# Kernel tuning notes

Hardware: AMD Instinct MI355X
Metric: run time of the kernel (lower is better)

Reference implementation:

```python
import jax, jax.numpy as jnp
import numpy as np

HEADS = 4


def setup_inputs() -> dict:
    key = jax.random.key(0)
    ks = jax.random.split(key, 6)
    b, c, d, h, w = 4, 512, 16, 16, 16
    x = jax.random.normal(ks[0], (b, c, d, h, w), dtype=jnp.float32)
    s = 0.02  # param init scale
    Wq = jax.random.normal(ks[1], (c, c), dtype=jnp.float32) * s
    Wk = jax.random.normal(ks[2], (c, c), dtype=jnp.float32) * s
    Wv = jax.random.normal(ks[3], (c, c), dtype=jnp.float32) * s
    Wproj = jax.random.normal(ks[4], (c, c), dtype=jnp.float32) * s
    bproj = jnp.zeros((c,), dtype=jnp.float32)
    return {"x": x, "Wq": Wq, "Wk": Wk, "Wv": Wv, "Wproj": Wproj, "bproj": bproj}


def reference(x, Wq, Wk, Wv, Wproj, bproj):
    b, c, d, h, w = x.shape
    N = d * h * w
    scale = (c // HEADS) ** -0.5  # module uses ch//heads for scale
    xf = x.reshape(b, c, N)  # (b, c, N)
    # 1x1 Conv1d == channel matmul
    q = jnp.einsum('oc,bcn->bon', Wq, xf)
    k = jnp.einsum('oc,bcn->bon', Wk, xf)
    v = jnp.einsum('oc,bcn->bon', Wv, xf)
    # Faithful to original (buggy) view: split SEQUENCE dim by heads -> (b, H, c, N//H)
    q = q.reshape(b, HEADS, c, N // HEADS)
    k = k.reshape(b, HEADS, c, N // HEADS)
    v = v.reshape(b, HEADS, c, N // HEADS)
    attn = jax.nn.softmax(jnp.einsum('bhqe,bhke->bhqk', q, k) * scale, axis=-1)
    out = jnp.einsum('bhqk,bhke->bhqe', attn, v)  # (b, H, c, N//H)
    out = jnp.swapaxes(out, 2, 3).reshape(b, c, N)  # matches transpose(2,3).view
    out = jnp.einsum('oc,bcn->bon', Wproj, out) + bproj[None, :, None]
    return out.reshape(b, c, d, h, w) + x
```

## Files before the change

kernel.cpp:

```cpp
#include <hip/hip_runtime.h>
#include <stdint.h>


typedef __attribute__((ext_vector_type(8))) short short8;
typedef __attribute__((ext_vector_type(4))) float f32x4;

typedef const __attribute__((address_space(1))) unsigned int* gas_ptr;
typedef __attribute__((address_space(3))) unsigned int* las_ptr;

#define ATTN_SCALE 0.08838834764831845f

__device__ __forceinline__ unsigned short f2bf(float f) {
    union { float f; unsigned int u; } c; c.f = f;
    unsigned int u = c.u;
    u += 0x7fffu + ((u >> 16) & 1u);
    return (unsigned short)(u >> 16);
}

__device__ __forceinline__ void gl_lds16(const void* g, void* l) {
    __builtin_amdgcn_global_load_lds((gas_ptr)(uintptr_t)g, (las_ptr)(uintptr_t)l,
                                     16, 0, 0);
}

template<int LDA, int LDB, int KDIM, bool PERMB = false>
__device__ __forceinline__ void mfma_core(
    const unsigned short* __restrict__ A,
    const unsigned short* __restrict__ B,
    int m0, int n0,
    unsigned short* __restrict__ sA, unsigned short* __restrict__ sB,
    f32x4 acc[4][4])
{
    const int tid  = threadIdx.x;
    const int lane = tid & 63, wave = tid >> 6;
    const int lr = lane >> 2, lc = lane & 3;
    const int lcs = lc ^ ((lr >> 1) & 3);
    const int wm = (wave & 1) * 64, wn = (wave >> 1) * 64;
    const int col = lane & 15, quad = lane >> 4;
    const int swz = (quad ^ ((col >> 1) & 3)) * 8;

    const unsigned short* ga = A + (size_t)(m0 + 32 * wave + lr) * LDA + lcs * 8;
    int rb0 = n0 + 32 * wave + lr;
    int rb1 = rb0 + 16;
    if (PERMB) {
        rb0 = 4 * (rb0 & 127) + (rb0 >> 7);
        rb1 = 4 * (rb1 & 127) + (rb1 >> 7);
    }
    const unsigned short* gb0 = B + (size_t)rb0 * LDB + lcs * 8;
    const unsigned short* gb1 = B + (size_t)rb1 * LDB + lcs * 8;

    const int wr0 = (32 * wave) * 32;
    const int wr1 = (32 * wave + 16) * 32;

    gl_lds16(ga,            sA + wr0);
    gl_lds16(ga + 16 * LDA, sA + wr1);
    gl_lds16(gb0,           sB + wr0);
    gl_lds16(gb1,           sB + wr1);

    constexpr int NK = KDIM / 32;
    for (int kk = 0; kk < NK; ++kk) {
        const int bo = (kk & 1) * 4096;
        if (kk + 1 < NK) {
            const int nb = ((kk + 1) & 1) * 4096;
            const int k0 = (kk + 1) * 32;
            gl_lds16(ga + k0,            sA + nb + wr0);
            gl_lds16(ga + k0 + 16 * LDA, sA + nb + wr1);
            gl_lds16(gb0 + k0,           sB + nb + wr0);
            gl_lds16(gb1 + k0,           sB + nb + wr1);
            asm volatile("s_waitcnt vmcnt(4)" ::: "memory");
        } else {
            asm volatile("s_waitcnt vmcnt(0)" ::: "memory");
        }
        __builtin_amdgcn_s_barrier();
        asm volatile("" ::: "memory");
        __builtin_amdgcn_sched_barrier(0);

        const unsigned short* bA = sA + bo;
        const unsigned short* bB = sB + bo;
        short8 af[4], bfv[4];
        #pragma unroll
        for (int i = 0; i < 4; ++i)
            af[i] = *(const short8*)&bA[(wm + i * 16 + col) * 32 + swz];
        #pragma unroll
        for (int j = 0; j < 4; ++j)
            bfv[j] = *(const short8*)&bB[(wn + j * 16 + col) * 32 + swz];
        #pragma unroll
        for (int i = 0; i < 4; ++i)
            #pragma unroll
            for (int j = 0; j < 4; ++j)
                acc[i][j] = __builtin_amdgcn_mfma_f32_16x16x32_bf16(
                    af[i], bfv[j], acc[i][j], 0, 0, 0);

        __builtin_amdgcn_s_barrier();
        asm volatile("" ::: "memory");
    }
}

__global__ __launch_bounds__(256)
void prep(const float* __restrict__ x,
          const float* __restrict__ Wq, const float* __restrict__ Wk,
          const float* __restrict__ Wv, const float* __restrict__ Wp,
          unsigned short* __restrict__ xT, unsigned short* __restrict__ Wb)
{
    if (blockIdx.z == 4) {
        const int idx = (blockIdx.y * 64 + blockIdx.x) * 256 + threadIdx.x;
        const int mat = idx >> 16;
        const int off = (idx & 65535) << 2;
        const float* src = (mat == 0 ? Wq : mat == 1 ? Wk : mat == 2 ? Wv : Wp) + off;
        const float4 f = *(const float4*)src;
        uint2 o;
        o.x = f2bf(f.x) | ((unsigned)f2bf(f.y) << 16);
        o.y = f2bf(f.z) | ((unsigned)f2bf(f.w) << 16);
        *(uint2*)&Wb[mat * 262144 + off] = o;
        return;
    }
    const int b = blockIdx.z;
    const int l = threadIdx.x & 63, w = threadIdx.x >> 6;
    const int n  = blockIdx.x * 64 + l;
    const int c0 = blockIdx.y * 32 + w * 8;
    const float* xp = x + (size_t)b * 2097152 + (size_t)c0 * 4096 + n;
    unsigned int p[4];
    #pragma unroll
    for (int j = 0; j < 4; ++j) {
        const unsigned short a  = f2bf(xp[(2 * j)     * 4096]);
        const unsigned short bb = f2bf(xp[(2 * j + 1) * 4096]);
        p[j] = a | ((unsigned)bb << 16);
    }
    uint4 v; v.x = p[0]; v.y = p[1]; v.z = p[2]; v.w = p[3];
    *(uint4*)&xT[(size_t)b * 2097152 + (size_t)n * 512 + c0] = v;
}

__global__ __launch_bounds__(256)
void gemm_qkv(const unsigned short* __restrict__ Wb,
              const unsigned short* __restrict__ xT,
              unsigned short* __restrict__ qb, unsigned short* __restrict__ kb,
              unsigned short* __restrict__ vT)
{
    __shared__ unsigned short sT[128 * 136];
    unsigned short* sA = sT;
    unsigned short* sB = sT + 8192;

    const int z = blockIdx.z, wsel = z >> 2, b = z & 3;
    const unsigned short* A = Wb + wsel * 262144;
    const unsigned short* B = xT + (size_t)b * 2097152;
    const int m0 = blockIdx.y * 128, n0 = blockIdx.x * 128;

    f32x4 z4 = {0.f, 0.f, 0.f, 0.f};
    f32x4 acc[4][4];
    #pragma unroll
    for (int i = 0; i < 4; ++i)
        #pragma unroll
        for (int j = 0; j < 4; ++j) acc[i][j] = z4;

    mfma_core<512, 512, 512>(A, B, m0, n0, sA, sB, acc);

    __syncthreads();

    const int tid = threadIdx.x;
    const int lane = tid & 63, wave = tid >> 6;
    const int wm = (wave & 1) * 64, wn = (wave >> 1) * 64;
    const int col = lane & 15, quad = lane >> 4;
    const int h = m0 >> 7, s = n0 >> 10;

    if (wsel < 2) {
        #pragma unroll
        for (int i = 0; i < 4; ++i)
            #pragma unroll
            for (int r = 0; r < 4; ++r) {
                const int rr = wm + i * 16 + quad * 4 + r;
                #pragma unroll
                for (int j = 0; j < 4; ++j)
                    sT[rr * 136 + wn + j * 16 + col] = f2bf(acc[i][j][r]);
            }
        __syncthreads();
        unsigned short* C = (wsel == 0 ? qb : kb)
                          + (size_t)(b * 4 + h) * 524288;
        const int bKc = (n0 & 1023) >> 5;
        const int u = tid & 15, v = (tid >> 4) & 3, wv = tid >> 6;
        unsigned short* dst = C + (size_t)(s * 256 + bKc + wv) * 512
                            + (v * 16 + u) * 8;
        const unsigned short* src = sT + u * 136 + wv * 32 + v * 8;
        #pragma unroll
        for (int k = 0; k < 8; ++k)
            *(uint4*)(dst + k * 16384) = *(const uint4*)(src + k * 2176);
    } else {
        #pragma unroll
        for (int i = 0; i < 4; ++i)
            #pragma unroll
            for (int r = 0; r < 4; ++r) {
                const int rr = wm + i * 16 + quad * 4 + r;
                #pragma unroll
                for (int j = 0; j < 4; ++j)
                    sT[(wn + j * 16 + col) * 136 + rr] = f2bf(acc[i][j][r]);
            }
        __syncthreads();
        const int e0 = n0 & 1023;
        unsigned short* dstb = vT + (size_t)(b * 4 + h) * 524288;
        const int ce = tid & 15, j = tid >> 4;
        const size_t base = (size_t)((e0 >> 4) * 32 + s * 4 + (j >> 2)) * 512
                          + ((j & 3) * 16 + ce) * 8;
        const unsigned short* srcb = sT + ce * 136 + j * 8;
        #pragma unroll
        for (int Re = 0; Re < 8; ++Re)
            *(uint4*)&dstb[base + (size_t)Re * 16384]
                = *(const uint4*)&srcb[Re * 2176];
    }
}

__global__ __launch_bounds__(512)
void attn(const unsigned short* __restrict__ qb,
          const unsigned short* __restrict__ kb,
          const unsigned short* __restrict__ vTf,
          unsigned short* __restrict__ yT)
{
    __shared__ unsigned short Pl[32 * 520];
    __shared__ float red[2][32][8];
    const int d = blockIdx.x;
    const int flat = (d & 7) * 32 + (d >> 3);
    const int rg = flat & 15, z = flat >> 4;
    const int b = z >> 2, hh = z & 3;
    const unsigned short* Aq = qb + (size_t)z * 524288;
    const unsigned short* Bk = kb + (size_t)z * 524288;
    const unsigned short* Vz = vTf + (size_t)z * 524288;
    unsigned short* yTb = yT + (size_t)b * 2097152;

    const int tid = threadIdx.x;
    const int lane = tid & 63, w = tid >> 6;
    const int col = lane & 15, quad = lane >> 4;

    const unsigned short* ap0 = Aq + (size_t)((rg * 2 + 0) * 32) * 512 + lane * 8;
    const unsigned short* ap1 = Aq + (size_t)((rg * 2 + 1) * 32) * 512 + lane * 8;
    const unsigned short* bp0 = Bk + (size_t)((w * 4 + 0) * 32) * 512 + lane * 8;
    const unsigned short* bp1 = bp0 + 16384;
    const unsigned short* bp2 = bp0 + 32768;
    const unsigned short* bp3 = bp0 + 49152;

    f32x4 z4 = {0.f, 0.f, 0.f, 0.f};
    f32x4 acc[2][4];
    #pragma unroll
    for (int f = 0; f < 2; ++f)
        #pragma unroll
        for (int g = 0; g < 4; ++g) acc[f][g] = z4;

    #pragma unroll 4
    for (int kk = 0; kk < 32; ++kk) {
        const int o = kk * 512;
        const short8 af0 = *(const short8*)(ap0 + o);
        const short8 af1 = *(const short8*)(ap1 + o);
        short8 bf[4];
        bf[0] = *(const short8*)(bp0 + o);
        bf[1] = *(const short8*)(bp1 + o);
        bf[2] = *(const short8*)(bp2 + o);
        bf[3] = *(const short8*)(bp3 + o);
        #pragma unroll
        for (int g = 0; g < 4; ++g)
            acc[0][g] = __builtin_amdgcn_mfma_f32_16x16x32_bf16(
                af0, bf[g], acc[0][g], 0, 0, 0);
        #pragma unroll
        for (int g = 0; g < 4; ++g)
            acc[1][g] = __builtin_amdgcn_mfma_f32_16x16x32_bf16(
                af1, bf[g], acc[1][g], 0, 0, 0);
    }

    float mx[2][4];
    #pragma unroll
    for (int f = 0; f < 2; ++f)
        #pragma unroll
        for (int r = 0; r < 4; ++r) {
            float m = acc[f][0][r];
            #pragma unroll
            for (int g = 1; g < 4; ++g) m = fmaxf(m, acc[f][g][r]);
            #pragma unroll
            for (int s = 1; s < 16; s <<= 1) m = fmaxf(m, __shfl_xor(m, s));
            mx[f][r] = m;
        }
    if (col == 0) {
        #pragma unroll
        for (int f = 0; f < 2; ++f)
            #pragma unroll
            for (int r = 0; r < 4; ++r)
                red[0][f * 16 + quad * 4 + r][w] = mx[f][r];
    }
    __syncthreads();
    float sm[2][4];
    #pragma unroll
    for (int f = 0; f < 2; ++f)
        #pragma unroll
        for (int r = 0; r < 4; ++r) {
            const int row = f * 16 + quad * 4 + r;
            float m = red[0][row][0];
            #pragma unroll
            for (int t = 1; t < 8; ++t) m = fmaxf(m, red[0][row][t]);
            float s = 0.f;
            #pragma unroll
            for (int g = 0; g < 4; ++g) {
                const float e = __expf((acc[f][g][r] - m) * ATTN_SCALE);
                acc[f][g][r] = e;
                s += e;
            }
            #pragma unroll
            for (int t = 1; t < 16; t <<= 1) s += __shfl_xor(s, t);
            sm[f][r] = s;
        }
    if (col == 0) {
        #pragma unroll
        for (int f = 0; f < 2; ++f)
            #pragma unroll
            for (int r = 0; r < 4; ++r)
                red[1][f * 16 + quad * 4 + r][w] = sm[f][r];
    }
    __syncthreads();
    #pragma unroll
    for (int f = 0; f < 2; ++f)
        #pragma unroll
        for (int r = 0; r < 4; ++r) {
            const int row = f * 16 + quad * 4 + r;
            float tot = red[1][row][0];
            #pragma unroll
            for (int t = 1; t < 8; ++t) tot += red[1][row][t];
            const float inv = 1.f / tot;
            #pragma unroll
            for (int g = 0; g < 4; ++g)
                Pl[row * 520 + w * 64 + g * 16 + col] =
                    f2bf(acc[f][g][r] * inv);
        }
    __syncthreads();

    f32x4 accp[2][8];
    #pragma unroll
    for (int f = 0; f < 2; ++f)
        #pragma unroll
        for (int g2 = 0; g2 < 8; ++g2) accp[f][g2] = z4;

    #pragma unroll 2
    for (int Kc = 0; Kc < 16; ++Kc) {
        const short8 a0 = *(const short8*)&Pl[col * 520 + Kc * 32 + quad * 8];
        const short8 a1 = *(const short8*)&Pl[(16 + col) * 520 + Kc * 32 + quad * 8];
        short8 bv[8];
        #pragma unroll
        for (int g2 = 0; g2 < 8; ++g2)
            bv[g2] = *(const short8*)&Vz[(size_t)((w * 8 + g2) * 32 + Kc) * 512
                                         + lane * 8];
        #pragma unroll
        for (int g2 = 0; g2 < 8; ++g2) {
            accp[0][g2] = __builtin_amdgcn_mfma_f32_16x16x32_bf16(
                a0, bv[g2], accp[0][g2], 0, 0, 0);
            accp[1][g2] = __builtin_amdgcn_mfma_f32_16x16x32_bf16(
                a1, bv[g2], accp[1][g2], 0, 0, 0);
        }
    }
    __syncthreads();

    unsigned short* Ol = Pl;
    const int rl = tid >> 4, s8 = (tid >> 1) & 7, hw = tid & 1;
    const int qsem = ((rg & 3) << 7) + 4 * rl + (rg >> 2);
    const size_t nbase = (size_t)(s8 * 512 + qsem) * 512 + hh * 128;
    #pragma unroll
    for (int h2 = 0; h2 < 2; ++h2) {
        if ((w >> 2) == h2) {
            const int wl = w & 3;
            #pragma unroll
            for (int f = 0; f < 2; ++f)
                #pragma unroll
                for (int g2 = 0; g2 < 8; ++g2)
                    #pragma unroll
                    for (int r = 0; r < 4; ++r)
                        Ol[(f * 16 + quad * 4 + r) * 520
                           + wl * 128 + g2 * 16 + col] = f2bf(accp[f][g2][r]);
        }
        __syncthreads();
        #pragma unroll
        for (int v2 = 0; v2 < 4; ++v2) {
            const int cdb = hw * 32 + v2 * 8;
            unsigned int p[4];
            #pragma unroll
            for (int t = 0; t < 4; ++t) {
                const unsigned int a  = Ol[rl * 520 + s8 + 8 * (cdb + 2 * t)];
                const unsigned int bb = Ol[rl * 520 + s8 + 8 * (cdb + 2 * t + 1)];
                p[t] = a | (bb << 16);
            }
            uint4 o; o.x = p[0]; o.y = p[1]; o.z = p[2]; o.w = p[3];
            *(uint4*)&yTb[nbase + h2 * 64 + cdb] = o;
        }
        __syncthreads();
    }
}

__global__ __launch_bounds__(256)
void gemm_proj(const unsigned short* __restrict__ Wpb,
               const unsigned short* __restrict__ yT,
               const float* __restrict__ bias, const float* __restrict__ x,
               float* __restrict__ out)
{
    __shared__ unsigned short sA[2 * 128 * 32], sB[2 * 128 * 32];
    const int b = blockIdx.z;
    const unsigned short* B = yT + (size_t)b * 2097152;
    const int m0 = blockIdx.y * 128, n0 = blockIdx.x * 128;

    f32x4 z4 = {0.f, 0.f, 0.f, 0.f};
    f32x4 acc[4][4];
    #pragma unroll
    for (int i = 0; i < 4; ++i)
        #pragma unroll
        for (int j = 0; j < 4; ++j) acc[i][j] = z4;

    mfma_core<512, 512, 512>(Wpb, B, m0, n0, sA, sB, acc);

    const int lane = threadIdx.x & 63, wave = threadIdx.x >> 6;
    const int wm = (wave & 1) * 64, wn = (wave >> 1) * 64;
    const int col = lane & 15, quad = lane >> 4;
    const size_t boff = (size_t)b * 2097152;
    #pragma unroll
    for (int i = 0; i < 4; ++i)
        #pragma unroll
        for (int r = 0; r < 4; ++r) {
            const int row = m0 + wm + i * 16 + quad * 4 + r;
            const float bi = bias[row];
            #pragma unroll
            for (int j = 0; j < 4; ++j) {
                const size_t idx = boff + (size_t)row * 4096 + n0 + wn + j * 16 + col;
                out[idx] = acc[i][j][r] + bi + x[idx];
            }
        }
}

extern "C" void kernel_launch(void* const* d_in, const int* in_sizes, int n_in,
                              void* d_out, int out_size, void* d_ws, size_t ws_size,
                              hipStream_t stream) {
    const float* x     = (const float*)d_in[0];
    const float* Wq    = (const float*)d_in[1];
    const float* Wk    = (const float*)d_in[2];
    const float* Wv    = (const float*)d_in[3];
    const float* Wproj = (const float*)d_in[4];
    const float* bproj = (const float*)d_in[5];
    float* out = (float*)d_out;

    char* w = (char*)d_ws;
    unsigned short* xT = (unsigned short*)(w + 0);
    unsigned short* qb = (unsigned short*)(w + 16777216);
    unsigned short* kb = (unsigned short*)(w + 33554432);
    unsigned short* vT = (unsigned short*)(w + 50331648);
    unsigned short* Wb = (unsigned short*)(w + 109051904);
    unsigned short* yT = xT;

    prep        <<<dim3(64, 16, 5),  256, 0, stream>>>(x, Wq, Wk, Wv, Wproj, xT, Wb);
    gemm_qkv    <<<dim3(32, 4, 12),  256, 0, stream>>>(Wb, xT, qb, kb, vT);
    attn        <<<dim3(256),        512, 0, stream>>>(qb, kb, vT, yT);
    gemm_proj   <<<dim3(32, 4, 4),   256, 0, stream>>>(Wb + 3 * 262144, yT, bproj, x, out);
}
```

Before: 192.6 us.

## Stage Q tile in LDS, prefetch V across softmax, double-buffer PV loads

In the attention kernel, the Q tile is now copied into shared memory once per block with direct global-to-LDS loads, so the eight waves no longer each fetch it from global memory. The first V fragments are issued before the softmax reductions, and the PV loop is double-buffered so the next V chunk loads while the current MFMAs run. The P matrix is written into shared memory in a fragment-ordered layout so each lane reads its A operand with one contiguous vector load. This hides global memory latency and cuts redundant Q traffic, at the cost of extra LDS (about 64KB more) and more registers, which could lower occupancy.

```diff
diff --git a/kernel.cpp b/kernel.cpp
--- a/kernel.cpp
+++ b/kernel.cpp
@@ -212,7 +212,8 @@
           const unsigned short* __restrict__ vTf,
           unsigned short* __restrict__ yT)
 {
-    __shared__ unsigned short Pl[32 * 520];
+    __shared__ unsigned short sAq[32 * 1024];
+    __shared__ unsigned short Pl[16640];
     __shared__ float red[2][32][8];
     const int d = blockIdx.x;
     const int flat = (d & 7) * 32 + (d >> 3);
@@ -227,13 +228,22 @@
     const int lane = tid & 63, w = tid >> 6;
     const int col = lane & 15, quad = lane >> 4;
 
-    const unsigned short* ap0 = Aq + (size_t)((rg * 2 + 0) * 32) * 512 + lane * 8;
-    const unsigned short* ap1 = Aq + (size_t)((rg * 2 + 1) * 32) * 512 + lane * 8;
+    {
+        const unsigned short* gsrc = Aq + (size_t)(rg * 2 * 32) * 512 + lane * 8;
+        #pragma unroll
+        for (int i = 0; i < 8; ++i)
+            gl_lds16(gsrc + (i * 8 + w) * 512, sAq + (i * 8 + w) * 512);
+    }
+
     const unsigned short* bp0 = Bk + (size_t)((w * 4 + 0) * 32) * 512 + lane * 8;
     const unsigned short* bp1 = bp0 + 16384;
     const unsigned short* bp2 = bp0 + 32768;
     const unsigned short* bp3 = bp0 + 49152;
 
+    asm volatile("s_waitcnt vmcnt(0)" ::: "memory");
+    __builtin_amdgcn_s_barrier();
+    asm volatile("" ::: "memory");
+
     f32x4 z4 = {0.f, 0.f, 0.f, 0.f};
     f32x4 acc[2][4];
     #pragma unroll
@@ -244,8 +254,8 @@
     #pragma unroll 4
     for (int kk = 0; kk < 32; ++kk) {
         const int o = kk * 512;
-        const short8 af0 = *(const short8*)(ap0 + o);
-        const short8 af1 = *(const short8*)(ap1 + o);
+        const short8 af0 = *(const short8*)&sAq[o + lane * 8];
+        const short8 af1 = *(const short8*)&sAq[16384 + o + lane * 8];
         short8 bf[4];
         bf[0] = *(const short8*)(bp0 + o);
         bf[1] = *(const short8*)(bp1 + o);
@@ -261,6 +271,11 @@
                 af1, bf[g], acc[1][g], 0, 0, 0);
     }
 
+    short8 bvA[8], bvB[8];
+    #pragma unroll
+    for (int g2 = 0; g2 < 8; ++g2)
+        bvA[g2] = *(const short8*)&Vz[(size_t)((w * 8 + g2) * 32) * 512 + lane * 8];
+
     float mx[2][4];
     #pragma unroll
     for (int f = 0; f < 2; ++f)
@@ -320,7 +335,9 @@
             const float inv = 1.f / tot;
             #pragma unroll
             for (int g = 0; g < 4; ++g)
-                Pl[row * 520 + w * 64 + g * 16 + col] =
+                Pl[(f * 16 + w * 2 + (g >> 1)) * 512
+                   + ((g & 1) * 2 + (col >> 3)) * 128
+                   + (quad * 4 + r) * 8 + (col & 7)] =
                     f2bf(acc[f][g][r] * inv);
         }
     __syncthreads();
@@ -331,21 +348,39 @@
         #pragma unroll
         for (int g2 = 0; g2 < 8; ++g2) accp[f][g2] = z4;
 
-    #pragma unroll 2
-    for (int Kc = 0; Kc < 16; ++Kc) {
-        const short8 a0 = *(const short8*)&Pl[col * 520 + Kc * 32 + quad * 8];
-        const short8 a1 = *(const short8*)&Pl[(16 + col) * 520 + Kc * 32 + quad * 8];
-        short8 bv[8];
+    #pragma unroll
+    for (int Kc = 0; Kc < 16; Kc += 2) {
         #pragma unroll
         for (int g2 = 0; g2 < 8; ++g2)
-            bv[g2] = *(const short8*)&Vz[(size_t)((w * 8 + g2) * 32 + Kc) * 512
-                                         + lane * 8];
-        #pragma unroll
-        for (int g2 = 0; g2 < 8; ++g2) {
-            accp[0][g2] = __builtin_amdgcn_mfma_f32_16x16x32_bf16(
-                a0, bv[g2], accp[0][g2], 0, 0, 0);
-            accp[1][g2] = __builtin_amdgcn_mfma_f32_16x16x32_bf16(
-                a1, bv[g2], accp[1][g2], 0, 0, 0);
+            bvB[g2] = *(const short8*)&Vz[(size_t)((w * 8 + g2) * 32 + Kc + 1) * 512
+                                          + lane * 8];
+        {
+            const short8 a0 = *(const short8*)&Pl[Kc * 512 + lane * 8];
+            const short8 a1 = *(const short8*)&Pl[(16 + Kc) * 512 + lane * 8];
+            #pragma unroll
+            for (int g2 = 0; g2 < 8; ++g2) {
+                accp[0][g2] = __builtin_amdgcn_mfma_f32_16x16x32_bf16(
+                    a0, bvA[g2], accp[0][g2], 0, 0, 0);
+                accp[1][g2] = __builtin_amdgcn_mfma_f32_16x16x32_bf16(
+                    a1, bvA[g2], accp[1][g2], 0, 0, 0);
+            }
+        }
+        if (Kc + 2 < 16) {
+            #pragma unroll
+            for (int g2 = 0; g2 < 8; ++g2)
+                bvA[g2] = *(const short8*)&Vz[(size_t)((w * 8 + g2) * 32 + Kc + 2) * 512
+                                              + lane * 8];
+        }
+        {
+            const short8 a2 = *(const short8*)&Pl[(Kc + 1) * 512 + lane * 8];
+            const short8 a3 = *(const short8*)&Pl[(16 + Kc + 1) * 512 + lane * 8];
+            #pragma unroll
+            for (int g2 = 0; g2 < 8; ++g2) {
+                accp[0][g2] = __builtin_amdgcn_mfma_f32_16x16x32_bf16(
+                    a2, bvB[g2], accp[0][g2], 0, 0, 0);
+                accp[1][g2] = __builtin_amdgcn_mfma_f32_16x16x32_bf16(
+                    a3, bvB[g2], accp[1][g2], 0, 0, 0);
+            }
         }
     }
     __syncthreads();
```

Result: no change. 189.2 us (-1.8%).
